# Optimization experiments

Hardware: AMD Instinct MI355X
Metric: run time of the kernel (lower is better)

Reference implementation:

```python
import jax, jax.numpy as jnp
import numpy as np

N, E, C = 50000, 10000, 500
NNZ = 400000
IN_DIM, EDGE_DIM, NODE_DIM, COMP_DIM = 128, 128, 128, 128


def _glorot(key, shape):
    fan = shape[0] + shape[1]
    return jax.random.normal(key, shape, jnp.float32) * (2.0 / fan) ** 0.5


def _seg_mean(vals, idx, num):
    # mean aggregation over segments (scatter-add + count normalize)
    s = jax.ops.segment_sum(vals, idx, num_segments=num)
    cnt = jax.ops.segment_sum(jnp.ones((idx.shape[0], 1), vals.dtype), idx, num_segments=num)
    return s / jnp.maximum(cnt, 1.0)


def _prelu(v, a):
    return jnp.where(v >= 0, v, a * v)


def _conv(x, ni, ei, ec_e, ec_c, nc_n, nc_c, n_nodes, n_edges, n_comps,
          Wne, Wen, Wec, Wnc, a):
    # node -> hyperedge message passing
    e = _seg_mean((x @ Wne)[ni], ei, n_edges)            # [E, edge_dim]
    e_act = _prelu(e, a)
    # hyperedge -> node
    n = _seg_mean((e_act @ Wen)[ei], ni, n_nodes)        # [N, node_dim]
    # edge -> component and node -> component
    c = _seg_mean((e_act @ Wec)[ec_e], ec_c, n_comps) + \
        _seg_mean((x @ Wnc)[nc_n], nc_c, n_comps)        # [C, comp_dim]
    return n, e, c


def setup_inputs() -> dict:
    key = jax.random.key(0)
    ks = jax.random.split(key, 16)
    x = jax.random.normal(ks[0], (N, IN_DIM), jnp.float32)
    hyperedge_index = jnp.stack([
        jax.random.randint(ks[1], (NNZ,), 0, N),
        jax.random.randint(ks[2], (NNZ,), 0, E),
    ])
    hyperedge_component_index = jnp.stack([
        jnp.arange(E), jax.random.randint(ks[3], (E,), 0, C)])
    node_component_index = jnp.stack([
        jnp.arange(N), jax.random.randint(ks[4], (N,), 0, C)])
    return dict(
        x=x,
        hyperedge_index=hyperedge_index,
        hyperedge_component_index=hyperedge_component_index,
        node_component_index=node_component_index,
        num_nodes=N, num_edges=E, num_components=C,
        W_ne0=_glorot(ks[5], (IN_DIM, EDGE_DIM)),
        W_en0=_glorot(ks[6], (EDGE_DIM, NODE_DIM)),
        W_ec0=_glorot(ks[7], (EDGE_DIM, COMP_DIM)),
        W_nc0=_glorot(ks[8], (IN_DIM, COMP_DIM)),
        W_ne1=_glorot(ks[9], (NODE_DIM, EDGE_DIM)),
        W_en1=_glorot(ks[10], (EDGE_DIM, NODE_DIM)),
        W_ec1=_glorot(ks[11], (EDGE_DIM, COMP_DIM)),
        W_nc1=_glorot(ks[12], (NODE_DIM, COMP_DIM)),
        prelu_a=jnp.array(0.25, jnp.float32),
    )


def reference(x, hyperedge_index, hyperedge_component_index, node_component_index,
              num_nodes, num_edges, num_components,
              W_ne0, W_en0, W_ec0, W_nc0, W_ne1, W_en1, W_ec1, W_nc1, prelu_a):
    ni, ei = hyperedge_index[0], hyperedge_index[1]
    ec_e, ec_c = hyperedge_component_index[0], hyperedge_component_index[1]
    nc_n, nc_c = node_component_index[0], node_component_index[1]
    layers = [(W_ne0, W_en0, W_ec0, W_nc0), (W_ne1, W_en1, W_ec1, W_nc1)]
    e_out = c_out = None
    for Wne, Wen, Wec, Wnc in layers:
        n_out, e_out, c_out = _conv(x, ni, ei, ec_e, ec_c, nc_n, nc_c,
                                    num_nodes, num_edges, num_components,
                                    Wne, Wen, Wec, Wnc, prelu_a)
        x = _prelu(n_out, prelu_a)  # HyperEncoder applies act between/after layers
    return (x, e_out, c_out)
```

## Files before the change

kernel.cpp:

```cpp
#include <hip/hip_runtime.h>
#include <stdint.h>

typedef unsigned int u32;
typedef _Float16 f16;
typedef f16 half8 __attribute__((ext_vector_type(8)));
typedef float f32x4 __attribute__((ext_vector_type(4)));
#define TS 4096
#define KB2 256
#define CH 2048

__device__ __forceinline__ float bflo(u32 u) { return __uint_as_float(u << 16); }
__device__ __forceinline__ float bfhi(u32 u) { return __uint_as_float(u & 0xffff0000u); }
__device__ __forceinline__ u32 f2bf(float x) {
    u32 u = __float_as_uint(x);
    return (u + 0x7fffu + ((u >> 16) & 1u)) >> 16;
}
__device__ __forceinline__ u32 pack2(float a, float b) { return f2bf(a) | (f2bf(b) << 16); }

__device__ __forceinline__ int bstart2(int b, int total) {
    return (int)(((unsigned long long)b * (u32)total + KB2 - 1) / KB2);
}

__device__ __forceinline__ int blk_exscan(int v, int& total) {
    __shared__ int ws[5];
    int t = threadIdx.x, lane = t & 63, w = t >> 6;
    int inc = v;
    for (int d = 1; d < 64; d <<= 1) { int u = __shfl_up(inc, d, 64); if (lane >= d) inc += u; }
    __syncthreads();
    if (lane == 63) ws[w] = inc;
    __syncthreads();
    if (t == 0) { int acc = 0; for (int i = 0; i < 4; ++i) { int x = ws[i]; ws[i] = acc; acc += x; } ws[4] = acc; }
    __syncthreads();
    total = ws[4];
    return ws[w] + (inc - v);
}

#define ACC8(v) do { \
    a[0] += bflo((v).x); a[1] += bfhi((v).x); a[2] += bflo((v).y); a[3] += bfhi((v).y); \
    a[4] += bflo((v).z); a[5] += bfhi((v).z); a[6] += bflo((v).w); a[7] += bfhi((v).w); } while (0)

__device__ __forceinline__ void seg_mean8(const u32* __restrict__ in,
                                          const int* __restrict__ items,
                                          const int* __restrict__ off,
                                          int nseg, int nrows, int seg, float a[8]) {
    int lane = threadIdx.x & 63;
    int rs = lane >> 4;
    int cc = lane & 15;
#pragma unroll
    for (int i = 0; i < 8; ++i) a[i] = 0.f;
    int s0 = 0, s1 = 0;
    if (seg < nseg) { s0 = off[seg]; s1 = off[seg + 1]; }
    const uint4* rows = (const uint4*)in;
    int base = s0;
    for (; base + 16 <= s1; base += 16) {
        u32 r0 = (u32)items[base + rs];
        u32 r1 = (u32)items[base + 4 + rs];
        u32 r2 = (u32)items[base + 8 + rs];
        u32 r3 = (u32)items[base + 12 + rs];
        r0 = (r0 < (u32)nrows) ? r0 : 0u;
        r1 = (r1 < (u32)nrows) ? r1 : 0u;
        r2 = (r2 < (u32)nrows) ? r2 : 0u;
        r3 = (r3 < (u32)nrows) ? r3 : 0u;
        uint4 v0 = rows[(size_t)r0 * 16 + cc];
        uint4 v1 = rows[(size_t)r1 * 16 + cc];
        uint4 v2 = rows[(size_t)r2 * 16 + cc];
        uint4 v3 = rows[(size_t)r3 * 16 + cc];
        ACC8(v0); ACC8(v1); ACC8(v2); ACC8(v3);
    }
    for (; base + 8 <= s1; base += 8) {
        u32 r0 = (u32)items[base + rs];
        u32 r1 = (u32)items[base + 4 + rs];
        r0 = (r0 < (u32)nrows) ? r0 : 0u;
        r1 = (r1 < (u32)nrows) ? r1 : 0u;
        uint4 v0 = rows[(size_t)r0 * 16 + cc];
        uint4 v1 = rows[(size_t)r1 * 16 + cc];
        ACC8(v0); ACC8(v1);
    }
    int idx = base + rs;
    if (idx < s1) {
        u32 r = (u32)items[idx]; r = (r < (u32)nrows) ? r : 0u;
        uint4 v = rows[(size_t)r * 16 + cc];
        ACC8(v);
    }
    idx += 4;
    if (idx < s1) {
        u32 r = (u32)items[idx]; r = (r < (u32)nrows) ? r : 0u;
        uint4 v = rows[(size_t)r * 16 + cc];
        ACC8(v);
    }
#pragma unroll
    for (int i = 0; i < 8; ++i) {
        a[i] += __shfl_xor(a[i], 16, 64);
        a[i] += __shfl_xor(a[i], 32, 64);
    }
    float inv = 1.f / fmaxf((float)(s1 - s0), 1.f);
#pragma unroll
    for (int i = 0; i < 8; ++i) a[i] *= inv;
}

__device__ __forceinline__ void agg4_body(const u32* __restrict__ in,
                                          const int* __restrict__ items,
                                          const int* __restrict__ off,
                                          float* __restrict__ out_f32,
                                          u32* __restrict__ out_bf,
                                          int nseg, int nrows, int do_prelu,
                                          const float* __restrict__ alpha_p, int seg) {
    if (seg >= nseg) return;
    int lane = threadIdx.x & 63;
    int rs = lane >> 4;
    int cc = lane & 15;
    float a[8];
    seg_mean8(in, items, off, nseg, nrows, seg, a);
    if (do_prelu) {
        float al = *alpha_p;
#pragma unroll
        for (int i = 0; i < 8; ++i) a[i] = (a[i] >= 0.f) ? a[i] : al * a[i];
    }
    if (rs == 0) {
        if (out_f32) {
            float* o = out_f32 + ((size_t)seg << 7) + cc * 8;
            *(float4*)o       = make_float4(a[0], a[1], a[2], a[3]);
            *(float4*)(o + 4) = make_float4(a[4], a[5], a[6], a[7]);
        }
        if (out_bf) {
            uint4 pk;
            pk.x = pack2(a[0], a[1]); pk.y = pack2(a[2], a[3]);
            pk.z = pack2(a[4], a[5]); pk.w = pack2(a[6], a[7]);
            *(uint4*)(out_bf + ((size_t)seg << 6) + cc * 4) = pk;
        }
    }
}

__global__ __launch_bounds__(256) void k_front(
        const int* __restrict__ ni, const int* __restrict__ ei,
        const int* __restrict__ nc_c, const int* __restrict__ ec_c,
        int* __restrict__ bcntE, int* __restrict__ bcntN,
        int* __restrict__ cnt_cn, int* __restrict__ cnt_ce,
        int nnz, int n, int e, int nbh,
        int* __restrict__ ticket,
        int* __restrict__ basesE, int* __restrict__ basesN,
        int* __restrict__ bcur_e, int* __restrict__ bcur_n,
        int* __restrict__ off_cn, int* __restrict__ off_ce,
        int* __restrict__ cur_cn, int* __restrict__ cur_ce, int c,
        const float* __restrict__ W0, const float* __restrict__ W1,
        const float* __restrict__ W2, const float* __restrict__ W3,
        const float* __restrict__ W4, const float* __restrict__ W5,
        f16* __restrict__ wt6) {
    int t = threadIdx.x;
    int b = blockIdx.x;
    if (b >= nbh) {
        int gid = (b - nbh) * 256 + t;
        if (gid >= 6 * 2048) return;
        int m = gid >> 11;
        int rem = gid & 2047;
        int cq = rem >> 4;
        int s = rem & 15;
        const float* W = (m == 0) ? W0 : (m == 1) ? W1 : (m == 2) ? W2 :
                         (m == 3) ? W3 : (m == 4) ? W4 : W5;
        int khi = ((s & 7) ^ (cq & 7)) | (s & 8);
        int k0 = khi << 3;
        union { f16 h[8]; uint4 v; } u;
#pragma unroll
        for (int j = 0; j < 8; ++j) u.h[j] = (f16)W[((k0 + j) << 7) + cq];
        *(uint4*)(wt6 + ((size_t)m << 14) + (cq << 7) + (s << 3)) = u.v;
        return;
    }
    __shared__ int hE[KB2], hN[KB2];
    __shared__ int lastflag;
    hE[t] = 0; hN[t] = 0;
    __syncthreads();
    int base = b * CH;
    int lim = base + CH; if (lim > nnz) lim = nnz;
    for (int i = base + t; i < lim; i += 256) {
        u32 v = (u32)ni[i], eg = (u32)ei[i];
        if (v >= (u32)n) v = 0;
        if (eg >= (u32)e) eg = 0;
        atomicAdd(&hE[(int)(((unsigned long long)eg * KB2) / (u32)e)], 1);
        atomicAdd(&hN[(int)(((unsigned long long)v  * KB2) / (u32)n)], 1);
    }
    __syncthreads();
    if (hE[t]) atomicAdd(&bcntE[t], hE[t]);
    if (hN[t]) atomicAdd(&bcntN[t], hN[t]);
    int gid = b * 256 + t, stride = nbh * 256;
    for (int j = gid; j < n + e; j += stride) {
        if (j < n) atomicAdd(&cnt_cn[nc_c[j]], 1);
        else       atomicAdd(&cnt_ce[ec_c[j - n]], 1);
    }
    __syncthreads();
    if (t == 0) {
        __threadfence();
        lastflag = (atomicAdd(ticket, 1) == nbh - 1);
    }
    __syncthreads();
    if (!lastflag) return;
    __threadfence();
    int tot;
    int v = bcntE[t];
    int ex = blk_exscan(v, tot);
    basesE[t] = ex; bcur_e[t] = ex;
    if (t == 0) basesE[KB2] = tot;
    v = bcntN[t];
    ex = blk_exscan(v, tot);
    basesN[t] = ex; bcur_n[t] = ex;
    if (t == 0) basesN[KB2] = tot;
    int i0 = 2 * t, i1 = 2 * t + 1;
    int v0 = (i0 < c) ? cnt_cn[i0] : 0;
    int v1 = (i1 < c) ? cnt_cn[i1] : 0;
    ex = blk_exscan(v0 + v1, tot);
    if (i0 < c) { off_cn[i0] = ex;      cur_cn[i0] = ex; }
    if (i1 < c) { off_cn[i1] = ex + v0; cur_cn[i1] = ex + v0; }
    if (t == 0) off_cn[c] = tot;
    v0 = (i0 < c) ? cnt_ce[i0] : 0;
    v1 = (i1 < c) ? cnt_ce[i1] : 0;
    ex = blk_exscan(v0 + v1, tot);
    if (i0 < c) { off_ce[i0] = ex;      cur_ce[i0] = ex; }
    if (i1 < c) { off_ce[i1] = ex + v0; cur_ce[i1] = ex + v0; }
    if (t == 0) off_ce[c] = tot;
}

__global__ __launch_bounds__(256) void k_part_a(
        const int* __restrict__ ni, const int* __restrict__ ei,
        int* __restrict__ bcur_e, int* __restrict__ bcur_n,
        u32* __restrict__ stg_e, u32* __restrict__ stg_n,
        const int* __restrict__ nc_n, const int* __restrict__ nc_c,
        const int* __restrict__ ec_e, const int* __restrict__ ec_c,
        int* __restrict__ cur_cn, int* __restrict__ cur_ce,
        int* __restrict__ csr_cn, int* __restrict__ csr_ce,
        const float2* __restrict__ xin, u32* __restrict__ xout, int npairs,
        int nnz, int n, int e, int nbh) {
    __shared__ u32 pk[CH];
    __shared__ unsigned short bb[CH];
    __shared__ int hist[KB2];
    __shared__ int gb[KB2];
    int t = threadIdx.x;
    int bx = blockIdx.x;
    if (bx >= 2 * nbh) {
        int j = (bx - 2 * nbh) * 256 + t;
        if (j < npairs) { float2 v = xin[j]; xout[j] = pack2(v.x, v.y); }
        return;
    }
    int side = bx >= nbh;
    int pb = side ? bx - nbh : bx;
    int base = pb * CH;
    int cnt  = nnz - base; if (cnt > CH) cnt = CH;
    for (int i = t; i < KB2; i += 256) hist[i] = 0;
    __syncthreads();
    u32 total = side ? (u32)n : (u32)e;
    for (int i = t; i < cnt; i += 256) {
        int v = ni[base + i], eg = ei[base + i];
        u32 key = side ? (u32)v : (u32)eg;
        u32 pay = side ? (u32)eg : (u32)v;
        if (key >= total) key = 0;
        u32 b = (u32)(((unsigned long long)key * KB2) / total);
        pk[i] = side ? (pay | (key << 14)) : (pay | (key << 16));
        bb[i] = (unsigned short)b;
        atomicAdd(&hist[b], 1);
    }
    __syncthreads();
    int* cursor = side ? bcur_n : bcur_e;
    u32* stg    = side ? stg_n  : stg_e;
    if (t < KB2) {
        int h = hist[t];
        gb[t] = h ? atomicAdd(&cursor[t], h) : 0;
        hist[t] = 0;
    }
    __syncthreads();
    for (int i = t; i < cnt; i += 256) {
        int b = bb[i];
        int r = atomicAdd(&hist[b], 1);
        stg[gb[b] + r] = pk[i];
    }
    int gid = pb * 256 + t;
    int stride = nbh * 256;
    if (side == 0) {
        for (int j = gid; j < e; j += stride) { int c = ec_c[j]; csr_ce[atomicAdd(&cur_ce[c], 1)] = ec_e[j]; }
    } else {
        for (int j = gid; j < n; j += stride) { int c = nc_c[j]; csr_cn[atomicAdd(&cur_cn[c], 1)] = nc_n[j]; }
    }
}

__global__ __launch_bounds__(256) void k_part_b2(
        const u32* __restrict__ stg_e, const u32* __restrict__ stg_n,
        const int* __restrict__ basesE, const int* __restrict__ basesN,
        int* __restrict__ off_e, int* __restrict__ off_n,
        int* __restrict__ csr_e, int* __restrict__ csr_n, int e, int n) {
    __shared__ int lcnt[256];
    int b = blockIdx.x, t = threadIdx.x;
    const u32* stg; const int* bases; int* off; int* csr; int total; int shift; u32 mask;
    if (b < KB2) { stg = stg_e; bases = basesE; off = off_e; csr = csr_e; total = e; shift = 16; mask = 0xFFFFu; }
    else { b -= KB2; stg = stg_n; bases = basesN; off = off_n; csr = csr_n; total = n; shift = 14; mask = 0x3FFFu; }
    int lo = bstart2(b, total), hi = bstart2(b + 1, total);
    int nid = hi - lo;
    int sbase = bases[b], send = bases[b + 1];
    lcnt[t] = 0;
    __syncthreads();
    for (int i = sbase + t; i < send; i += 256) {
        int key = (int)(stg[i] >> shift);
        atomicAdd(&lcnt[key - lo], 1);
    }
    __syncthreads();
    int cval = (t < nid) ? lcnt[t] : 0;
    int tot;
    int ex = blk_exscan(cval, tot);
    int cursor = sbase + ex;
    if (t < nid) { off[lo + t] = cursor; lcnt[t] = cursor; }
    if (t == 0 && hi == total) off[total] = send;
    __syncthreads();
    for (int i = sbase + t; i < send; i += 256) {
        u32 s = stg[i];
        int key = (int)(s >> shift);
        int pay = (int)(s & mask);
        int p = atomicAdd(&lcnt[key - lo], 1);
        csr[p] = pay;
    }
}

__global__ void k_cvt(const float2* __restrict__ in, u32* __restrict__ out, int npairs) {
    int j = blockIdx.x * blockDim.x + threadIdx.x;
    if (j < npairs) { float2 v = in[j]; out[j] = pack2(v.x, v.y); }
}

__global__ void k_hist_fb(const int* __restrict__ ni, const int* __restrict__ ei,
                          const int* __restrict__ nc_c, const int* __restrict__ ec_c,
                          int* __restrict__ deg_e, int* __restrict__ deg_n,
                          int* __restrict__ cnt_cn, int* __restrict__ cnt_ce,
                          int nnz, int n, int e) {
    int j = blockIdx.x * blockDim.x + threadIdx.x;
    if (j < nnz) {
        atomicAdd(&deg_e[ei[j]], 1);
        atomicAdd(&deg_n[ni[j]], 1);
    }
    if (j < n) atomicAdd(&cnt_cn[nc_c[j]], 1);
    if (j < e) atomicAdd(&cnt_ce[ec_c[j]], 1);
}

__device__ __forceinline__ void scan_sel(int b, int t0, int t01, int t012,
        const int* c0, int* o0, int* u0, int n0,
        const int* c1, int* o1, int* u1, int n1,
        const int* c2, int* o2, int* u2, int n2,
        const int* c3, int* o3, int* u3, int n3,
        const int*& cnt, int*& off, int*& cur, int& n, int& tile) {
    if (b < t0)        { cnt = c0; off = o0; cur = u0; n = n0; tile = b; }
    else if (b < t01)  { cnt = c1; off = o1; cur = u1; n = n1; tile = b - t0; }
    else if (b < t012) { cnt = c2; off = o2; cur = u2; n = n2; tile = b - t01; }
    else               { cnt = c3; off = o3; cur = u3; n = n3; tile = b - t012; }
}

__global__ void k_scan_p1(const int* c0, int n0, const int* c1, int n1,
                          const int* c2, int n2, const int* c3, int n3,
                          int t0, int t01, int t012, int* __restrict__ tilesum) {
    __shared__ int ws[4];
    int b = blockIdx.x;
    const int* cnt; int* off; int* cur; int n; int tile;
    scan_sel(b, t0, t01, t012, c0, nullptr, nullptr, n0, c1, nullptr, nullptr, n1,
             c2, nullptr, nullptr, n2, c3, nullptr, nullptr, n3, cnt, off, cur, n, tile);
    int base = tile * TS + threadIdx.x * 16;
    int s = 0;
#pragma unroll
    for (int i = 0; i < 16; ++i) { int idx = base + i; if (idx < n) s += cnt[idx]; }
    for (int d = 32; d; d >>= 1) s += __shfl_xor(s, d, 64);
    int lane = threadIdx.x & 63, w = threadIdx.x >> 6;
    if (lane == 0) ws[w] = s;
    __syncthreads();
    if (threadIdx.x == 0) tilesum[b] = ws[0] + ws[1] + ws[2] + ws[3];
}

__global__ void k_scan_p2(const int* __restrict__ tilesum, int* __restrict__ tilebase,
                          int t0, int t01, int t012, int t0123,
                          int* o0, int n0, int* o1, int n1, int* o2, int n2, int* o3, int n3) {
    if (threadIdx.x != 0 || blockIdx.x != 0) return;
    int carry = 0;
    for (int b = 0;    b < t0;    ++b) { tilebase[b] = carry; carry += tilesum[b]; } o0[n0] = carry;
    carry = 0;
    for (int b = t0;   b < t01;   ++b) { tilebase[b] = carry; carry += tilesum[b]; } o1[n1] = carry;
    carry = 0;
    for (int b = t01;  b < t012;  ++b) { tilebase[b] = carry; carry += tilesum[b]; } o2[n2] = carry;
    carry = 0;
    for (int b = t012; b < t0123; ++b) { tilebase[b] = carry; carry += tilesum[b]; } o3[n3] = carry;
}

__global__ void k_scan_p3(const int* c0, int* o0, int* u0, int n0,
                          const int* c1, int* o1, int* u1, int n1,
                          const int* c2, int* o2, int* u2, int n2,
                          const int* c3, int* o3, int* u3, int n3,
                          int t0, int t01, int t012, const int* __restrict__ tilebase) {
    __shared__ int wsum[4];
    int b = blockIdx.x;
    const int* cnt; int* off; int* cur; int n; int tile;
    scan_sel(b, t0, t01, t012, c0, o0, u0, n0, c1, o1, u1, n1,
             c2, o2, u2, n2, c3, o3, u3, n3, cnt, off, cur, n, tile);
    int lane = threadIdx.x & 63, w = threadIdx.x >> 6;
    int base = tile * TS + threadIdx.x * 16;
    int vals[16];
    int s = 0;
#pragma unroll
    for (int i = 0; i < 16; ++i) { int idx = base + i; int v = (idx < n) ? cnt[idx] : 0; vals[i] = v; s += v; }
    int inc = s;
    for (int d = 1; d < 64; d <<= 1) { int u = __shfl_up(inc, d, 64); if (lane >= d) inc += u; }
    if (lane == 63) wsum[w] = inc;
    __syncthreads();
    if (threadIdx.x == 0) {
        int acc = tilebase[b];
        for (int i = 0; i < 4; ++i) { int t = wsum[i]; wsum[i] = acc; acc += t; }
    }
    __syncthreads();
    int ex = wsum[w] + (inc - s);
#pragma unroll
    for (int i = 0; i < 16; ++i) {
        int idx = base + i;
        if (idx < n) { off[idx] = ex; cur[idx] = ex; }
        ex += vals[i];
    }
}

__global__ void k_scatter(const int* __restrict__ ni, const int* __restrict__ ei,
                          const int* __restrict__ nc_n, const int* __restrict__ nc_c,
                          const int* __restrict__ ec_e, const int* __restrict__ ec_c,
                          int* __restrict__ cur_e, int* __restrict__ cur_n,
                          int* __restrict__ cur_cn, int* __restrict__ cur_ce,
                          int* __restrict__ csr_e, int* __restrict__ csr_n,
                          int* __restrict__ csr_cn, int* __restrict__ csr_ce,
                          int nnz, int n, int e) {
    int j = blockIdx.x * blockDim.x + threadIdx.x;
    if (j < nnz) {
        int v = ni[j], eg = ei[j];
        csr_e[atomicAdd(&cur_e[eg], 1)] = v;
        csr_n[atomicAdd(&cur_n[v], 1)] = eg;
    }
    if (j < n) { int c = nc_c[j]; csr_cn[atomicAdd(&cur_cn[c], 1)] = nc_n[j]; }
    if (j < e) { int c = ec_c[j]; csr_ce[atomicAdd(&cur_ce[c], 1)] = ec_e[j]; }
}

__global__ __launch_bounds__(256) void k_agg4(
        const u32* __restrict__ in, const int* __restrict__ items,
        const int* __restrict__ off, float* __restrict__ out_f32,
        u32* __restrict__ out_bf,
        int nseg, int nrows, int do_prelu, const float* __restrict__ alpha_p) {
    int seg = blockIdx.x * (blockDim.x >> 6) + (threadIdx.x >> 6);
    agg4_body(in, items, off, out_f32, out_bf, nseg, nrows, do_prelu, alpha_p, seg);
}

__global__ __launch_bounds__(256) void k_agg4h(
        const u32* __restrict__ in, const int* __restrict__ items,
        const int* __restrict__ off, f16* __restrict__ outh,
        int nseg, int nrows) {
    int seg = blockIdx.x * (blockDim.x >> 6) + (threadIdx.x >> 6);
    if (seg >= nseg) return;
    float a[8];
    seg_mean8(in, items, off, nseg, nrows, seg, a);
    int lane = threadIdx.x & 63, rs = lane >> 4, cc = lane & 15;
    if (rs == 0) {
        union { f16 h[8]; uint4 v; } u;
#pragma unroll
        for (int i = 0; i < 8; ++i) u.h[i] = (f16)a[i];
        *(uint4*)(outh + ((size_t)seg << 7) + cc * 8) = u.v;
    }
}

__global__ __launch_bounds__(256) void k_agg_final(
        const u32* __restrict__ ybf, const int* __restrict__ csr_n, const int* __restrict__ off_n,
        float* __restrict__ out_x, int n, int e,
        const u32* __restrict__ eactbf, const int* __restrict__ csr_ce, const int* __restrict__ off_ce,
        float* __restrict__ ca_e,
        const u32* __restrict__ x1bf, const int* __restrict__ csr_cn, const int* __restrict__ off_cn,
        float* __restrict__ ca_n,
        int c, int nblkN, int ncb, const float* __restrict__ alpha_p) {
    int b = blockIdx.x;
    int wv = threadIdx.x >> 6;
    if (b < nblkN) {
        agg4_body(ybf, csr_n, off_n, out_x, nullptr, n, e, 1, alpha_p, b * 4 + wv);
    } else if (b < nblkN + ncb) {
        agg4_body(eactbf, csr_ce, off_ce, ca_e, nullptr, c, e, 0, nullptr, (b - nblkN) * 4 + wv);
    } else {
        agg4_body(x1bf, csr_cn, off_cn, ca_n, nullptr, c, n, 0, nullptr, (b - nblkN - ncb) * 4 + wv);
    }
}

__global__ __launch_bounds__(256) void k_mlp_mfma(
        const f16* __restrict__ Ah,
        const f16* __restrict__ W1t, const f16* __restrict__ W2t,
        float* __restrict__ out_raw, u32* __restrict__ out_actbf,
        u32* __restrict__ out_ybf, int M, const float* __restrict__ alpha_p) {
    __shared__ f16 As[32 * 128];
    __shared__ f16 Wt[128 * 128];
    int t = threadIdx.x;
    int rb = blockIdx.x * 32;
    float al = *alpha_p;
    {
        const uint4* src = (const uint4*)W1t;
        uint4* dst = (uint4*)Wt;
        for (int i = t; i < 2048; i += 256) dst[i] = src[i];
    }
    {
        const uint4* Ag = (const uint4*)Ah;
        for (int i = t; i < 512; i += 256) {
            int r = i >> 4, s = i & 15;
            int row = rb + r;
            uint4 v = make_uint4(0u, 0u, 0u, 0u);
            if (row < M) v = Ag[(size_t)row * 16 + s];
            *(uint4*)((char*)As + (r << 8) + ((s << 4) ^ ((r & 7) << 4))) = v;
        }
    }
    __syncthreads();

    int lane = t & 63, wv = t >> 6;
    int r0  = (wv >> 1) << 4;
    int ctb = (wv & 1) << 2;
    int frow = lane & 15;
    int fk = (lane >> 4) << 3;
    int rl0 = r0 + ((lane >> 4) << 2);
    int ar = r0 + frow;
    int asw = (ar & 7) << 4;

    f32x4 acc[4] = {{0.f,0.f,0.f,0.f},{0.f,0.f,0.f,0.f},{0.f,0.f,0.f,0.f},{0.f,0.f,0.f,0.f}};
#pragma unroll
    for (int ks = 0; ks < 4; ++ks) {
        int kb2 = (ks * 32 + fk) << 1;
        half8 a = *(const half8*)((const char*)As + (ar << 8) + (kb2 ^ asw));
#pragma unroll
        for (int j = 0; j < 4; ++j) {
            int c = ((ctb + j) << 4) + frow;
            half8 b = *(const half8*)((const char*)Wt + (c << 8) + (kb2 ^ ((c & 7) << 4)));
            acc[j] = __builtin_amdgcn_mfma_f32_16x16x32_f16(a, b, acc[j], 0, 0, 0);
        }
    }
    __syncthreads();
    {
        const uint4* src = (const uint4*)W2t;
        uint4* dst = (uint4*)Wt;
        for (int i = t; i < 2048; i += 256) dst[i] = src[i];
    }
#pragma unroll
    for (int j = 0; j < 4; ++j) {
        int c = ((ctb + j) << 4) + frow;
#pragma unroll
        for (int rg = 0; rg < 4; ++rg) {
            int rl = rl0 + rg;
            int row = rb + rl;
            float ev = acc[j][rg];
            if (out_raw != nullptr && row < M) out_raw[((size_t)row << 7) + c] = ev;
            float av = (ev >= 0.f) ? ev : al * ev;
            float po = __shfl_xor(av, 1, 64);
            if (out_actbf != nullptr && (frow & 1) == 0 && row < M)
                out_actbf[((size_t)row << 6) + (c >> 1)] = pack2(av, po);
            *(f16*)((char*)As + (rl << 8) + (((c << 1)) ^ ((rl & 7) << 4))) = (f16)av;
        }
    }
    __syncthreads();
    f32x4 acc2[4] = {{0.f,0.f,0.f,0.f},{0.f,0.f,0.f,0.f},{0.f,0.f,0.f,0.f},{0.f,0.f,0.f,0.f}};
#pragma unroll
    for (int ks = 0; ks < 4; ++ks) {
        int kb2 = (ks * 32 + fk) << 1;
        half8 a = *(const half8*)((const char*)As + (ar << 8) + (kb2 ^ asw));
#pragma unroll
        for (int j = 0; j < 4; ++j) {
            int c = ((ctb + j) << 4) + frow;
            half8 b = *(const half8*)((const char*)Wt + (c << 8) + (kb2 ^ ((c & 7) << 4)));
            acc2[j] = __builtin_amdgcn_mfma_f32_16x16x32_f16(a, b, acc2[j], 0, 0, 0);
        }
    }
#pragma unroll
    for (int j = 0; j < 4; ++j) {
        int c = ((ctb + j) << 4) + frow;
#pragma unroll
        for (int rg = 0; rg < 4; ++rg) {
            int rl = rl0 + rg;
            int row = rb + rl;
            float yv = acc2[j][rg];
            float po = __shfl_xor(yv, 1, 64);
            if ((frow & 1) == 0 && row < M)
                out_ybf[((size_t)row << 6) + (c >> 1)] = pack2(yv, po);
        }
    }
}

__global__ __launch_bounds__(256) void k_gemm_mfma(
        const float* __restrict__ A1, const f16* __restrict__ W1t,
        const float* __restrict__ A2, const f16* __restrict__ W2t,
        float* __restrict__ out, int M) {
    __shared__ f16 Asd[2][32 * 128];
    __shared__ f16 Wt[128 * 128];
    int t = threadIdx.x;
    int rb = blockIdx.x * 32;
    {
        const uint4* src = (const uint4*)W1t;
        uint4* dst = (uint4*)Wt;
        for (int i = t; i < 2048; i += 256) dst[i] = src[i];
    }
    for (int p = 0; p < 2; ++p) {
        const float* Ap = p ? A2 : A1;
        for (int i = t; i < 32 * 32; i += 256) {
            int r = i >> 5, dc = i & 31;
            int row = rb + r;
            float4 v = make_float4(0.f, 0.f, 0.f, 0.f);
            if (row < M) v = *(const float4*)(Ap + ((size_t)row << 7) + dc * 4);
            f16* q = (f16*)((char*)Asd[p] + (r << 8) + ((dc << 3) ^ ((r & 7) << 4)));
            q[0] = (f16)v.x; q[1] = (f16)v.y; q[2] = (f16)v.z; q[3] = (f16)v.w;
        }
    }
    __syncthreads();

    int lane = t & 63, wv = t >> 6;
    int r0  = (wv >> 1) << 4;
    int ctb = (wv & 1) << 2;
    int frow = lane & 15;
    int fk = (lane >> 4) << 3;
    int rl0 = r0 + ((lane >> 4) << 2);
    int ar = r0 + frow;
    int asw = (ar & 7) << 4;

    f32x4 acc[4] = {{0.f,0.f,0.f,0.f},{0.f,0.f,0.f,0.f},{0.f,0.f,0.f,0.f},{0.f,0.f,0.f,0.f}};
#pragma unroll
    for (int ks = 0; ks < 4; ++ks) {
        int kb2 = (ks * 32 + fk) << 1;
        half8 a = *(const half8*)((const char*)Asd[0] + (ar << 8) + (kb2 ^ asw));
#pragma unroll
        for (int j = 0; j < 4; ++j) {
            int c = ((ctb + j) << 4) + frow;
            half8 b = *(const half8*)((const char*)Wt + (c << 8) + (kb2 ^ ((c & 7) << 4)));
            acc[j] = __builtin_amdgcn_mfma_f32_16x16x32_f16(a, b, acc[j], 0, 0, 0);
        }
    }
    __syncthreads();
    {
        const uint4* src = (const uint4*)W2t;
        uint4* dst = (uint4*)Wt;
        for (int i = t; i < 2048; i += 256) dst[i] = src[i];
    }
    __syncthreads();
#pragma unroll
    for (int ks = 0; ks < 4; ++ks) {
        int kb2 = (ks * 32 + fk) << 1;
        half8 a = *(const half8*)((const char*)Asd[1] + (ar << 8) + (kb2 ^ asw));
#pragma unroll
        for (int j = 0; j < 4; ++j) {
            int c = ((ctb + j) << 4) + frow;
            half8 b = *(const half8*)((const char*)Wt + (c << 8) + (kb2 ^ ((c & 7) << 4)));
            acc[j] = __builtin_amdgcn_mfma_f32_16x16x32_f16(a, b, acc[j], 0, 0, 0);
        }
    }
#pragma unroll
    for (int j = 0; j < 4; ++j) {
        int c = ((ctb + j) << 4) + frow;
#pragma unroll
        for (int rg = 0; rg < 4; ++rg) {
            int row = rb + rl0 + rg;
            if (row < M) out[((size_t)row << 7) + c] = acc[j][rg];
        }
    }
}

extern "C" void kernel_launch(void* const* d_in, const int* in_sizes, int n_in,
                              void* d_out, int out_size, void* d_ws, size_t ws_size,
                              hipStream_t stream) {
    const int N   = in_sizes[0] / 128;
    const int NNZ = in_sizes[1] / 2;
    const int E   = in_sizes[2] / 2;
    const int C   = 500;

    const float* x0 = (const float*)d_in[0];
    const int* ni   = (const int*)d_in[1];
    const int* ei   = ni + NNZ;
    const int* ec_e = (const int*)d_in[2];
    const int* ec_c = ec_e + E;
    const int* nc_n = (const int*)d_in[3];
    const int* nc_c = nc_n + N;
    const float* Wne0 = (const float*)d_in[7];
    const float* Wen0 = (const float*)d_in[8];
    const float* Wne1 = (const float*)d_in[11];
    const float* Wen1 = (const float*)d_in[12];
    const float* Wec1 = (const float*)d_in[13];
    const float* Wnc1 = (const float*)d_in[14];
    const float* alpha = (const float*)d_in[15];

    float* out_x = (float*)d_out;
    float* out_e = out_x + (size_t)N * 128;
    float* out_c = out_e + (size_t)E * 128;

    char* w = (char*)d_ws;
    auto alloc = [&](size_t bytes) { char* p = w; w += (bytes + 255) & ~(size_t)255; return p; };
    int* zgrp   = (int*)alloc((size_t)(2 * KB2 + 2 * C + 1) * 4);
    int* bcntE  = zgrp;
    int* bcntN  = zgrp + KB2;
    int* cnt_cn = zgrp + 2 * KB2;
    int* cnt_ce = zgrp + 2 * KB2 + C;
    int* ticket = zgrp + 2 * KB2 + 2 * C;
    int* off_e  = (int*)alloc((size_t)(E + 1) * 4);
    int* off_n  = (int*)alloc((size_t)(N + 1) * 4);
    int* off_cn = (int*)alloc((size_t)(C + 1) * 4);
    int* off_ce = (int*)alloc((size_t)(C + 1) * 4);
    int* cur_cn = (int*)alloc((size_t)C * 4);
    int* cur_ce = (int*)alloc((size_t)C * 4);
    int* csr_e  = (int*)alloc((size_t)NNZ * 4);
    int* csr_n  = (int*)alloc((size_t)NNZ * 4);
    int* csr_cn = (int*)alloc((size_t)N * 4);
    int* csr_ce = (int*)alloc((size_t)E * 4);
    int* basesE = (int*)alloc((size_t)(KB2 + 1) * 4);
    int* basesN = (int*)alloc((size_t)(KB2 + 1) * 4);
    int* bcur_e = (int*)alloc(KB2 * 4);
    int* bcur_n = (int*)alloc(KB2 * 4);
    u32* stg_e  = (u32*)alloc((size_t)NNZ * 4);
    u32* stg_n  = (u32*)alloc((size_t)NNZ * 4);
    u32* xbf    = (u32*)alloc((size_t)N * 64 * 4);
    u32* x1bf   = (u32*)alloc((size_t)N * 64 * 4);
    u32* ybf    = (u32*)alloc((size_t)E * 64 * 4);
    u32* eactbf = (u32*)alloc((size_t)E * 64 * 4);
    f16* xah    = (f16*)alloc((size_t)E * 128 * 2);
    float* ca_e = (float*)alloc((size_t)C * 128 * 4);
    float* ca_n = (float*)alloc((size_t)C * 128 * 4);
    f16* wt6    = (f16*)alloc((size_t)6 * 16384 * 2);
    int* deg_e    = (int*)alloc((size_t)E * 4);
    int* deg_n    = (int*)alloc((size_t)N * 4);
    int* cur_e    = (int*)alloc((size_t)E * 4);
    int* cur_n    = (int*)alloc((size_t)N * 4);
    int* tilesum  = (int*)alloc(64 * 4);
    int* tilebase = (int*)alloc(64 * 4);

    const int th = 256;
    const int npairs = N * 64;
    const int nbh = (NNZ + CH - 1) / CH;
    const int nkc = (npairs + th - 1) / th;

    bool binned = (E <= 16384) && (N <= 65536) && (E >= KB2) && (N >= KB2) &&
                  ((N + KB2 - 1) / KB2 <= 256) && (C <= 512);
    const int nbh_eff = binned ? nbh : 0;

    hipMemsetAsync(zgrp, 0, (size_t)(2 * KB2 + 2 * C + 1) * 4, stream);
    k_front<<<nbh_eff + 48, 256, 0, stream>>>(
        ni, ei, nc_c, ec_c,
        bcntE, bcntN, cnt_cn, cnt_ce, NNZ, N, E, nbh_eff,
        ticket, basesE, basesN, bcur_e, bcur_n,
        off_cn, off_ce, cur_cn, cur_ce, C,
        Wne0, Wen0, Wne1, Wen1, Wec1, Wnc1, wt6);

    if (binned) {
        k_part_a<<<2 * nbh + nkc, 256, 0, stream>>>(
            ni, ei, bcur_e, bcur_n, stg_e, stg_n,
            nc_n, nc_c, ec_e, ec_c,
            cur_cn, cur_ce, csr_cn, csr_ce,
            (const float2*)x0, xbf, npairs, NNZ, N, E, nbh);
        k_part_b2<<<2 * KB2, 256, 0, stream>>>(stg_e, stg_n, basesE, basesN,
                                               off_e, off_n, csr_e, csr_n, E, N);
    } else {
        hipMemsetAsync(deg_e, 0, (size_t)E * 4, stream);
        hipMemsetAsync(deg_n, 0, (size_t)N * 4, stream);
        k_cvt<<<(npairs + th - 1) / th, th, 0, stream>>>((const float2*)x0, xbf, npairs);
        k_hist_fb<<<(NNZ > N + E ? NNZ : N + E) / th + 1, th, 0, stream>>>(
            ni, ei, nc_c, ec_c, deg_e, deg_n, cnt_cn, cnt_ce, NNZ, N, E);
        const int t0 = (E + TS - 1) / TS, t1 = (N + TS - 1) / TS;
        const int t2 = (C + TS - 1) / TS, t3 = (C + TS - 1) / TS;
        const int t01 = t0 + t1, t012 = t01 + t2, t0123 = t012 + t3;
        k_scan_p1<<<t0123, 256, 0, stream>>>(deg_e, E, deg_n, N, cnt_cn, C, cnt_ce, C,
                                             t0, t01, t012, tilesum);
        k_scan_p2<<<1, 64, 0, stream>>>(tilesum, tilebase, t0, t01, t012, t0123,
                                        off_e, E, off_n, N, off_cn, C, off_ce, C);
        k_scan_p3<<<t0123, 256, 0, stream>>>(deg_e, off_e, cur_e, E,
                                             deg_n, off_n, cur_n, N,
                                             cnt_cn, off_cn, cur_cn, C,
                                             cnt_ce, off_ce, cur_ce, C,
                                             t0, t01, t012, tilebase);
        k_scatter<<<(NNZ + th - 1) / th, th, 0, stream>>>(ni, ei, nc_n, nc_c, ec_e, ec_c,
                                                          cur_e, cur_n, cur_cn, cur_ce,
                                                          csr_e, csr_n, csr_cn, csr_ce, NNZ, N, E);
    }

    const int gmlp = (E + 31) / 32;
    k_agg4h<<<(E + 3) / 4, 256, 0, stream>>>(xbf, csr_e, off_e, xah, E, N);
    k_mlp_mfma<<<gmlp, 256, 0, stream>>>(xah, wt6, wt6 + 16384, nullptr, nullptr, ybf, E, alpha);
    k_agg4<<<(N + 3) / 4, 256, 0, stream>>>(ybf, csr_n, off_n, nullptr, x1bf, N, E, 1, alpha);
    k_agg4h<<<(E + 3) / 4, 256, 0, stream>>>(x1bf, csr_e, off_e, xah, E, N);
    k_mlp_mfma<<<gmlp, 256, 0, stream>>>(xah, wt6 + 2 * 16384, wt6 + 3 * 16384,
                                         out_e, eactbf, ybf, E, alpha);
    {
        const int nblkN = (N + 3) / 4;
        const int ncb   = (C + 3) / 4;
        k_agg_final<<<nblkN + 2 * ncb, 256, 0, stream>>>(
            ybf, csr_n, off_n, out_x, N, E,
            eactbf, csr_ce, off_ce, ca_e,
            x1bf,   csr_cn, off_cn, ca_n,
            C, nblkN, ncb, alpha);
    }
    k_gemm_mfma<<<(C + 31) / 32, 256, 0, stream>>>(ca_e, wt6 + 4 * 16384,
                                                   ca_n, wt6 + 5 * 16384, out_c, C);
}
```

Before: 263.2 us.

## Fuse back-half message-passing stages into one persistent cooperative kernel

Replaces the sequence of aggregation, MLP, and final GEMM launches with a single cooperative persistent kernel that loops over work items and uses grid-wide syncs between stages. It also moves the node-to-component aggregation earlier, overlapping it with the second edge aggregation, and adds nontemporal stores for the final outputs. The aim is to remove per-launch overhead and tail gaps between dependent kernels. In exchange, the grid is capped by occupancy at 4 blocks per CU, each grid.sync has a cost, and the work inside each stage loses the parallelism of a full oversubscribed launch.

```diff
diff --git a/kernel.cpp b/kernel.cpp
--- a/kernel.cpp
+++ b/kernel.cpp
@@ -1,5 +1,8 @@
 #include <hip/hip_runtime.h>
+#include <hip/hip_cooperative_groups.h>
 #include <stdint.h>
+
+namespace cg = cooperative_groups;
 
 typedef unsigned int u32;
 typedef _Float16 f16;
@@ -104,7 +107,8 @@
                                           float* __restrict__ out_f32,
                                           u32* __restrict__ out_bf,
                                           int nseg, int nrows, int do_prelu,
-                                          const float* __restrict__ alpha_p, int seg) {
+                                          const float* __restrict__ alpha_p, int seg,
+                                          int nt) {
     if (seg >= nseg) return;
     int lane = threadIdx.x & 63;
     int rs = lane >> 4;
@@ -119,8 +123,15 @@
     if (rs == 0) {
         if (out_f32) {
             float* o = out_f32 + ((size_t)seg << 7) + cc * 8;
-            *(float4*)o       = make_float4(a[0], a[1], a[2], a[3]);
-            *(float4*)(o + 4) = make_float4(a[4], a[5], a[6], a[7]);
+            f32x4 v0 = {a[0], a[1], a[2], a[3]};
+            f32x4 v1 = {a[4], a[5], a[6], a[7]};
+            if (nt) {
+                __builtin_nontemporal_store(v0, (f32x4*)o);
+                __builtin_nontemporal_store(v1, (f32x4*)(o + 4));
+            } else {
+                *(f32x4*)o = v0;
+                *(f32x4*)(o + 4) = v1;
+            }
         }
         if (out_bf) {
             uint4 pk;
@@ -129,6 +140,228 @@
             *(uint4*)(out_bf + ((size_t)seg << 6) + cc * 4) = pk;
         }
     }
+}
+
+__device__ __forceinline__ void aggh_body(const u32* __restrict__ in,
+                                          const int* __restrict__ items,
+                                          const int* __restrict__ off,
+                                          f16* __restrict__ outh,
+                                          int nseg, int nrows, int seg) {
+    if (seg >= nseg) return;
+    float a[8];
+    seg_mean8(in, items, off, nseg, nrows, seg, a);
+    int lane = threadIdx.x & 63, rs = lane >> 4, cc = lane & 15;
+    if (rs == 0) {
+        union { f16 h[8]; uint4 v; } u;
+#pragma unroll
+        for (int i = 0; i < 8; ++i) u.h[i] = (f16)a[i];
+        *(uint4*)(outh + ((size_t)seg << 7) + cc * 8) = u.v;
+    }
+}
+
+__device__ __forceinline__ void mlp_body(f16* As, f16* Wt, int rb,
+        const f16* __restrict__ Ah,
+        const f16* __restrict__ W1t, const f16* __restrict__ W2t,
+        float* __restrict__ out_raw, u32* __restrict__ out_actbf,
+        u32* __restrict__ out_ybf, int M, float al) {
+    int t = threadIdx.x;
+    __syncthreads();
+    {
+        const uint4* src = (const uint4*)W1t;
+        uint4* dst = (uint4*)Wt;
+        for (int i = t; i < 2048; i += 256) dst[i] = src[i];
+    }
+    {
+        const uint4* Ag = (const uint4*)Ah;
+        for (int i = t; i < 512; i += 256) {
+            int r = i >> 4, s = i & 15;
+            int row = rb + r;
+            uint4 v = make_uint4(0u, 0u, 0u, 0u);
+            if (row < M) v = Ag[(size_t)row * 16 + s];
+            *(uint4*)((char*)As + (r << 8) + ((s << 4) ^ ((r & 7) << 4))) = v;
+        }
+    }
+    __syncthreads();
+
+    int lane = t & 63, wv = t >> 6;
+    int r0  = (wv >> 1) << 4;
+    int ctb = (wv & 1) << 2;
+    int frow = lane & 15;
+    int fk = (lane >> 4) << 3;
+    int rl0 = r0 + ((lane >> 4) << 2);
+    int ar = r0 + frow;
+    int asw = (ar & 7) << 4;
+
+    f32x4 acc[4] = {{0.f,0.f,0.f,0.f},{0.f,0.f,0.f,0.f},{0.f,0.f,0.f,0.f},{0.f,0.f,0.f,0.f}};
+#pragma unroll
+    for (int ks = 0; ks < 4; ++ks) {
+        int kb2 = (ks * 32 + fk) << 1;
+        half8 a = *(const half8*)((const char*)As + (ar << 8) + (kb2 ^ asw));
+#pragma unroll
+        for (int j = 0; j < 4; ++j) {
+            int c = ((ctb + j) << 4) + frow;
+            half8 b = *(const half8*)((const char*)Wt + (c << 8) + (kb2 ^ ((c & 7) << 4)));
+            acc[j] = __builtin_amdgcn_mfma_f32_16x16x32_f16(a, b, acc[j], 0, 0, 0);
+        }
+    }
+    __syncthreads();
+    {
+        const uint4* src = (const uint4*)W2t;
+        uint4* dst = (uint4*)Wt;
+        for (int i = t; i < 2048; i += 256) dst[i] = src[i];
+    }
+#pragma unroll
+    for (int j = 0; j < 4; ++j) {
+        int c = ((ctb + j) << 4) + frow;
+#pragma unroll
+        for (int rg = 0; rg < 4; ++rg) {
+            int rl = rl0 + rg;
+            int row = rb + rl;
+            float ev = acc[j][rg];
+            if (out_raw != nullptr && row < M)
+                __builtin_nontemporal_store(ev, out_raw + ((size_t)row << 7) + c);
+            float av = (ev >= 0.f) ? ev : al * ev;
+            float po = __shfl_xor(av, 1, 64);
+            if (out_actbf != nullptr && (frow & 1) == 0 && row < M)
+                out_actbf[((size_t)row << 6) + (c >> 1)] = pack2(av, po);
+            *(f16*)((char*)As + (rl << 8) + (((c << 1)) ^ ((rl & 7) << 4))) = (f16)av;
+        }
+    }
+    __syncthreads();
+    f32x4 acc2[4] = {{0.f,0.f,0.f,0.f},{0.f,0.f,0.f,0.f},{0.f,0.f,0.f,0.f},{0.f,0.f,0.f,0.f}};
+#pragma unroll
+    for (int ks = 0; ks < 4; ++ks) {
+        int kb2 = (ks * 32 + fk) << 1;
+        half8 a = *(const half8*)((const char*)As + (ar << 8) + (kb2 ^ asw));
+#pragma unroll
+        for (int j = 0; j < 4; ++j) {
+            int c = ((ctb + j) << 4) + frow;
+            half8 b = *(const half8*)((const char*)Wt + (c << 8) + (kb2 ^ ((c & 7) << 4)));
+            acc2[j] = __builtin_amdgcn_mfma_f32_16x16x32_f16(a, b, acc2[j], 0, 0, 0);
+        }
+    }
+#pragma unroll
+    for (int j = 0; j < 4; ++j) {
+        int c = ((ctb + j) << 4) + frow;
+#pragma unroll
+        for (int rg = 0; rg < 4; ++rg) {
+            int rl = rl0 + rg;
+            int row = rb + rl;
+            float yv = acc2[j][rg];
+            float po = __shfl_xor(yv, 1, 64);
+            if ((frow & 1) == 0 && row < M)
+                out_ybf[((size_t)row << 6) + (c >> 1)] = pack2(yv, po);
+        }
+    }
+}
+
+__device__ __forceinline__ void gemm_body(f16* As, f16* Wt, int rb,
+        const float* __restrict__ A1, const f16* __restrict__ W1t,
+        const float* __restrict__ A2, const f16* __restrict__ W2t,
+        float* __restrict__ out, int M) {
+    int t = threadIdx.x, lane = t & 63, wv = t >> 6;
+    int r0 = (wv >> 1) << 4, ctb = (wv & 1) << 2;
+    int frow = lane & 15, fk = (lane >> 4) << 3;
+    int rl0 = r0 + ((lane >> 4) << 2);
+    int ar = r0 + frow, asw = (ar & 7) << 4;
+    f32x4 acc[4] = {{0.f,0.f,0.f,0.f},{0.f,0.f,0.f,0.f},{0.f,0.f,0.f,0.f},{0.f,0.f,0.f,0.f}};
+#pragma unroll 1
+    for (int p = 0; p < 2; ++p) {
+        const float* Ap = p ? A2 : A1;
+        const f16* Wp = p ? W2t : W1t;
+        __syncthreads();
+        {
+            const uint4* src = (const uint4*)Wp;
+            uint4* dst = (uint4*)Wt;
+            for (int i = t; i < 2048; i += 256) dst[i] = src[i];
+        }
+        for (int i = t; i < 32 * 32; i += 256) {
+            int r = i >> 5, dc = i & 31;
+            int row = rb + r;
+            float4 v = make_float4(0.f, 0.f, 0.f, 0.f);
+            if (row < M) v = *(const float4*)(Ap + ((size_t)row << 7) + dc * 4);
+            f16* q = (f16*)((char*)As + (r << 8) + ((dc << 3) ^ ((r & 7) << 4)));
+            q[0] = (f16)v.x; q[1] = (f16)v.y; q[2] = (f16)v.z; q[3] = (f16)v.w;
+        }
+        __syncthreads();
+#pragma unroll
+        for (int ks = 0; ks < 4; ++ks) {
+            int kb2 = (ks * 32 + fk) << 1;
+            half8 a = *(const half8*)((const char*)As + (ar << 8) + (kb2 ^ asw));
+#pragma unroll
+            for (int j = 0; j < 4; ++j) {
+                int c = ((ctb + j) << 4) + frow;
+                half8 b = *(const half8*)((const char*)Wt + (c << 8) + (kb2 ^ ((c & 7) << 4)));
+                acc[j] = __builtin_amdgcn_mfma_f32_16x16x32_f16(a, b, acc[j], 0, 0, 0);
+            }
+        }
+    }
+#pragma unroll
+    for (int j = 0; j < 4; ++j) {
+        int c = ((ctb + j) << 4) + frow;
+#pragma unroll
+        for (int rg = 0; rg < 4; ++rg) {
+            int row = rb + rl0 + rg;
+            if (row < M)
+                __builtin_nontemporal_store(acc[j][rg], out + ((size_t)row << 7) + c);
+        }
+    }
+}
+
+struct BackArgs {
+    const u32* xbf; u32* x1bf; u32* ybf; u32* eactbf; f16* xah;
+    const int* csr_e; const int* off_e;
+    const int* csr_n; const int* off_n;
+    const int* csr_cn; const int* off_cn;
+    const int* csr_ce; const int* off_ce;
+    const f16* wt6;
+    float* out_x; float* out_e; float* out_c;
+    float* ca_e; float* ca_n;
+    const float* alpha;
+    int N, E, C;
+};
+
+__global__ __launch_bounds__(256, 4) void k_back(BackArgs A) {
+    __shared__ f16 As[32 * 128];
+    __shared__ f16 Wt[128 * 128];
+    cg::grid_group grid = cg::this_grid();
+    int G = gridDim.x, bid = blockIdx.x;
+    int wv = threadIdx.x >> 6;
+    float al = *A.alpha;
+    const int EB = (A.E + 3) / 4, NB = (A.N + 3) / 4, CB = (A.C + 3) / 4;
+    const int GM = (A.E + 31) / 32, CG = (A.C + 31) / 32;
+
+    for (int vb = bid; vb < EB; vb += G)
+        aggh_body(A.xbf, A.csr_e, A.off_e, A.xah, A.E, A.N, vb * 4 + wv);
+    grid.sync();
+    for (int vb = bid; vb < GM; vb += G)
+        mlp_body(As, Wt, vb * 32, A.xah, A.wt6, A.wt6 + 16384,
+                 nullptr, nullptr, A.ybf, A.E, al);
+    grid.sync();
+    for (int vb = bid; vb < NB; vb += G)
+        agg4_body(A.ybf, A.csr_n, A.off_n, nullptr, A.x1bf, A.N, A.E, 1, A.alpha,
+                  vb * 4 + wv, 0);
+    grid.sync();
+    for (int vb = bid; vb < EB + CB; vb += G) {
+        if (vb < EB) aggh_body(A.x1bf, A.csr_e, A.off_e, A.xah, A.E, A.N, vb * 4 + wv);
+        else agg4_body(A.x1bf, A.csr_cn, A.off_cn, A.ca_n, nullptr, A.C, A.N, 0, A.alpha,
+                       (vb - EB) * 4 + wv, 0);
+    }
+    grid.sync();
+    for (int vb = bid; vb < GM; vb += G)
+        mlp_body(As, Wt, vb * 32, A.xah, A.wt6 + 2 * 16384, A.wt6 + 3 * 16384,
+                 A.out_e, A.eactbf, A.ybf, A.E, al);
+    grid.sync();
+    for (int vb = bid; vb < NB + CB; vb += G) {
+        if (vb < NB) agg4_body(A.ybf, A.csr_n, A.off_n, A.out_x, nullptr, A.N, A.E, 1,
+                               A.alpha, vb * 4 + wv, 1);
+        else agg4_body(A.eactbf, A.csr_ce, A.off_ce, A.ca_e, nullptr, A.C, A.E, 0,
+                       A.alpha, (vb - NB) * 4 + wv, 0);
+    }
+    grid.sync();
+    for (int vb = bid; vb < CG; vb += G)
+        gemm_body(As, Wt, vb * 32, A.ca_e, A.wt6 + 4 * 16384,
+                  A.ca_n, A.wt6 + 5 * 16384, A.out_c, A.C);
 }
 
 __global__ __launch_bounds__(256) void k_front(
@@ -437,7 +670,7 @@
         u32* __restrict__ out_bf,
         int nseg, int nrows, int do_prelu, const float* __restrict__ alpha_p) {
     int seg = blockIdx.x * (blockDim.x >> 6) + (threadIdx.x >> 6);
-    agg4_body(in, items, off, out_f32, out_bf, nseg, nrows, do_prelu, alpha_p, seg);
+    agg4_body(in, items, off, out_f32, out_bf, nseg, nrows, do_prelu, alpha_p, seg, 0);
 }
 
 __global__ __launch_bounds__(256) void k_agg4h(
@@ -445,16 +678,7 @@
         const int* __restrict__ off, f16* __restrict__ outh,
         int nseg, int nrows) {
     int seg = blockIdx.x * (blockDim.x >> 6) + (threadIdx.x >> 6);
-    if (seg >= nseg) return;
-    float a[8];
-    seg_mean8(in, items, off, nseg, nrows, seg, a);
-    int lane = threadIdx.x & 63, rs = lane >> 4, cc = lane & 15;
-    if (rs == 0) {
-        union { f16 h[8]; uint4 v; } u;
-#pragma unroll
-        for (int i = 0; i < 8; ++i) u.h[i] = (f16)a[i];
-        *(uint4*)(outh + ((size_t)seg << 7) + cc * 8) = u.v;
-    }
+    aggh_body(in, items, off, outh, nseg, nrows, seg);
 }
 
 __global__ __launch_bounds__(256) void k_agg_final(
@@ -468,11 +692,11 @@
     int b = blockIdx.x;
     int wv = threadIdx.x >> 6;
     if (b < nblkN) {
-        agg4_body(ybf, csr_n, off_n, out_x, nullptr, n, e, 1, alpha_p, b * 4 + wv);
+        agg4_body(ybf, csr_n, off_n, out_x, nullptr, n, e, 1, alpha_p, b * 4 + wv, 1);
     } else if (b < nblkN + ncb) {
-        agg4_body(eactbf, csr_ce, off_ce, ca_e, nullptr, c, e, 0, nullptr, (b - nblkN) * 4 + wv);
+        agg4_body(eactbf, csr_ce, off_ce, ca_e, nullptr, c, e, 0, nullptr, (b - nblkN) * 4 + wv, 0);
     } else {
-        agg4_body(x1bf, csr_cn, off_cn, ca_n, nullptr, c, n, 0, nullptr, (b - nblkN - ncb) * 4 + wv);
+        agg4_body(x1bf, csr_cn, off_cn, ca_n, nullptr, c, n, 0, nullptr, (b - nblkN - ncb) * 4 + wv, 0);
     }
 }
 
@@ -483,171 +707,16 @@
         u32* __restrict__ out_ybf, int M, const float* __restrict__ alpha_p) {
     __shared__ f16 As[32 * 128];
     __shared__ f16 Wt[128 * 128];
-    int t = threadIdx.x;
-    int rb = blockIdx.x * 32;
-    float al = *alpha_p;
-    {
-        const uint4* src = (const uint4*)W1t;
-        uint4* dst = (uint4*)Wt;
-        for (int i = t; i < 2048; i += 256) dst[i] = src[i];
-    }
-    {
-        const uint4* Ag = (const uint4*)Ah;
-        for (int i = t; i < 512; i += 256) {
-            int r = i >> 4, s = i & 15;
-            int row = rb + r;
-            uint4 v = make_uint4(0u, 0u, 0u, 0u);
-            if (row < M) v = Ag[(size_t)row * 16 + s];
-            *(uint4*)((char*)As + (r << 8) + ((s << 4) ^ ((r & 7) << 4))) = v;
-        }
-    }
-    __syncthreads();
-
-    int lane = t & 63, wv = t >> 6;
-    int r0  = (wv >> 1) << 4;
-    int ctb = (wv & 1) << 2;
-    int frow = lane & 15;
-    int fk = (lane >> 4) << 3;
-    int rl0 = r0 + ((lane >> 4) << 2);
-    int ar = r0 + frow;
-    int asw = (ar & 7) << 4;
-
-    f32x4 acc[4] = {{0.f,0.f,0.f,0.f},{0.f,0.f,0.f,0.f},{0.f,0.f,0.f,0.f},{0.f,0.f,0.f,0.f}};
-#pragma unroll
-    for (int ks = 0; ks < 4; ++ks) {
-        int kb2 = (ks * 32 + fk) << 1;
-        half8 a = *(const half8*)((const char*)As + (ar << 8) + (kb2 ^ asw));
-#pragma unroll
-        for (int j = 0; j < 4; ++j) {
-            int c = ((ctb + j) << 4) + frow;
-            half8 b = *(const half8*)((const char*)Wt + (c << 8) + (kb2 ^ ((c & 7) << 4)));
-            acc[j] = __builtin_amdgcn_mfma_f32_16x16x32_f16(a, b, acc[j], 0, 0, 0);
-        }
-    }
-    __syncthreads();
-    {
-        const uint4* src = (const uint4*)W2t;
-        uint4* dst = (uint4*)Wt;
-        for (int i = t; i < 2048; i += 256) dst[i] = src[i];
-    }
-#pragma unroll
-    for (int j = 0; j < 4; ++j) {
-        int c = ((ctb + j) << 4) + frow;
-#pragma unroll
-        for (int rg = 0; rg < 4; ++rg) {
-            int rl = rl0 + rg;
-            int row = rb + rl;
-            float ev = acc[j][rg];
-            if (out_raw != nullptr && row < M) out_raw[((size_t)row << 7) + c] = ev;
-            float av = (ev >= 0.f) ? ev : al * ev;
-            float po = __shfl_xor(av, 1, 64);
-            if (out_actbf != nullptr && (frow & 1) == 0 && row < M)
-                out_actbf[((size_t)row << 6) + (c >> 1)] = pack2(av, po);
-            *(f16*)((char*)As + (rl << 8) + (((c << 1)) ^ ((rl & 7) << 4))) = (f16)av;
-        }
-    }
-    __syncthreads();
-    f32x4 acc2[4] = {{0.f,0.f,0.f,0.f},{0.f,0.f,0.f,0.f},{0.f,0.f,0.f,0.f},{0.f,0.f,0.f,0.f}};
-#pragma unroll
-    for (int ks = 0; ks < 4; ++ks) {
-        int kb2 = (ks * 32 + fk) << 1;
-        half8 a = *(const half8*)((const char*)As + (ar << 8) + (kb2 ^ asw));
-#pragma unroll
-        for (int j = 0; j < 4; ++j) {
-            int c = ((ctb + j) << 4) + frow;
-            half8 b = *(const half8*)((const char*)Wt + (c << 8) + (kb2 ^ ((c & 7) << 4)));
-            acc2[j] = __builtin_amdgcn_mfma_f32_16x16x32_f16(a, b, acc2[j], 0, 0, 0);
-        }
-    }
-#pragma unroll
-    for (int j = 0; j < 4; ++j) {
-        int c = ((ctb + j) << 4) + frow;
-#pragma unroll
-        for (int rg = 0; rg < 4; ++rg) {
-            int rl = rl0 + rg;
-            int row = rb + rl;
-            float yv = acc2[j][rg];
-            float po = __shfl_xor(yv, 1, 64);
-            if ((frow & 1) == 0 && row < M)
-                out_ybf[((size_t)row << 6) + (c >> 1)] = pack2(yv, po);
-        }
-    }
+    mlp_body(As, Wt, blockIdx.x * 32, Ah, W1t, W2t, out_raw, out_actbf, out_ybf, M, *alpha_p);
 }
 
 __global__ __launch_bounds__(256) void k_gemm_mfma(
         const float* __restrict__ A1, const f16* __restrict__ W1t,
         const float* __restrict__ A2, const f16* __restrict__ W2t,
         float* __restrict__ out, int M) {
-    __shared__ f16 Asd[2][32 * 128];
+    __shared__ f16 As[32 * 128];
     __shared__ f16 Wt[128 * 128];
-    int t = threadIdx.x;
-    int rb = blockIdx.x * 32;
-    {
-        const uint4* src = (const uint4*)W1t;
-        uint4* dst = (uint4*)Wt;
-        for (int i = t; i < 2048; i += 256) dst[i] = src[i];
-    }
-    for (int p = 0; p < 2; ++p) {
-        const float* Ap = p ? A2 : A1;
-        for (int i = t; i < 32 * 32; i += 256) {
-            int r = i >> 5, dc = i & 31;
-            int row = rb + r;
-            float4 v = make_float4(0.f, 0.f, 0.f, 0.f);
-            if (row < M) v = *(const float4*)(Ap + ((size_t)row << 7) + dc * 4);
-            f16* q = (f16*)((char*)Asd[p] + (r << 8) + ((dc << 3) ^ ((r & 7) << 4)));
-            q[0] = (f16)v.x; q[1] = (f16)v.y; q[2] = (f16)v.z; q[3] = (f16)v.w;
-        }
-    }
-    __syncthreads();
-
-    int lane = t & 63, wv = t >> 6;
-    int r0  = (wv >> 1) << 4;
-    int ctb = (wv & 1) << 2;
-    int frow = lane & 15;
-    int fk = (lane >> 4) << 3;
-    int rl0 = r0 + ((lane >> 4) << 2);
-    int ar = r0 + frow;
-    int asw = (ar & 7) << 4;
-
-    f32x4 acc[4] = {{0.f,0.f,0.f,0.f},{0.f,0.f,0.f,0.f},{0.f,0.f,0.f,0.f},{0.f,0.f,0.f,0.f}};
-#pragma unroll
-    for (int ks = 0; ks < 4; ++ks) {
-        int kb2 = (ks * 32 + fk) << 1;
-        half8 a = *(const half8*)((const char*)Asd[0] + (ar << 8) + (kb2 ^ asw));
-#pragma unroll
-        for (int j = 0; j < 4; ++j) {
-            int c = ((ctb + j) << 4) + frow;
-            half8 b = *(const half8*)((const char*)Wt + (c << 8) + (kb2 ^ ((c & 7) << 4)));
-            acc[j] = __builtin_amdgcn_mfma_f32_16x16x32_f16(a, b, acc[j], 0, 0, 0);
-        }
-    }
-    __syncthreads();
-    {
-        const uint4* src = (const uint4*)W2t;
-        uint4* dst = (uint4*)Wt;
-        for (int i = t; i < 2048; i += 256) dst[i] = src[i];
-    }
-    __syncthreads();
-#pragma unroll
-    for (int ks = 0; ks < 4; ++ks) {
-        int kb2 = (ks * 32 + fk) << 1;
-        half8 a = *(const half8*)((const char*)Asd[1] + (ar << 8) + (kb2 ^ asw));
-#pragma unroll
-        for (int j = 0; j < 4; ++j) {
-            int c = ((ctb + j) << 4) + frow;
-            half8 b = *(const half8*)((const char*)Wt + (c << 8) + (kb2 ^ ((c & 7) << 4)));
-            acc[j] = __builtin_amdgcn_mfma_f32_16x16x32_f16(a, b, acc[j], 0, 0, 0);
-        }
-    }
-#pragma unroll
-    for (int j = 0; j < 4; ++j) {
-        int c = ((ctb + j) << 4) + frow;
-#pragma unroll
-        for (int rg = 0; rg < 4; ++rg) {
-            int row = rb + rl0 + rg;
-            if (row < M) out[((size_t)row << 7) + c] = acc[j][rg];
-        }
-    }
+    gemm_body(As, Wt, blockIdx.x * 32, A1, W1t, A2, W2t, out, M);
 }
 
 extern "C" void kernel_launch(void* const* d_in, const int* in_sizes, int n_in,
@@ -764,22 +833,55 @@
                                                           csr_e, csr_n, csr_cn, csr_ce, NNZ, N, E);
     }
 
-    const int gmlp = (E + 31) / 32;
-    k_agg4h<<<(E + 3) / 4, 256, 0, stream>>>(xbf, csr_e, off_e, xah, E, N);
-    k_mlp_mfma<<<gmlp, 256, 0, stream>>>(xah, wt6, wt6 + 16384, nullptr, nullptr, ybf, E, alpha);
-    k_agg4<<<(N + 3) / 4, 256, 0, stream>>>(ybf, csr_n, off_n, nullptr, x1bf, N, E, 1, alpha);
-    k_agg4h<<<(E + 3) / 4, 256, 0, stream>>>(x1bf, csr_e, off_e, xah, E, N);
-    k_mlp_mfma<<<gmlp, 256, 0, stream>>>(xah, wt6 + 2 * 16384, wt6 + 3 * 16384,
-                                         out_e, eactbf, ybf, E, alpha);
-    {
-        const int nblkN = (N + 3) / 4;
-        const int ncb   = (C + 3) / 4;
-        k_agg_final<<<nblkN + 2 * ncb, 256, 0, stream>>>(
-            ybf, csr_n, off_n, out_x, N, E,
-            eactbf, csr_ce, off_ce, ca_e,
-            x1bf,   csr_cn, off_cn, ca_n,
-            C, nblkN, ncb, alpha);
-    }
-    k_gemm_mfma<<<(C + 31) / 32, 256, 0, stream>>>(ca_e, wt6 + 4 * 16384,
-                                                   ca_n, wt6 + 5 * 16384, out_c, C);
-}
+    static int coopG = -1;
+    if (coopG < 0) {
+        int dev = 0, sup = 0, ncu = 0, nb = 0;
+        hipGetDevice(&dev);
+        hipDeviceGetAttribute(&sup, hipDeviceAttributeCooperativeLaunch, dev);
+        hipDeviceGetAttribute(&ncu, hipDeviceAttributeMultiprocessorCount, dev);
+        hipError_t oe = hipOccupancyMaxActiveBlocksPerMultiprocessor(
+            &nb, (const void*)k_back, 256, 0);
+        coopG = (sup && oe == hipSuccess && nb > 0 && ncu > 0) ? nb * ncu : 0;
+    }
+
+    bool ran_coop = false;
+    if (coopG > 0) {
+        BackArgs ba;
+        ba.xbf = xbf; ba.x1bf = x1bf; ba.ybf = ybf; ba.eactbf = eactbf; ba.xah = xah;
+        ba.csr_e = csr_e; ba.off_e = off_e;
+        ba.csr_n = csr_n; ba.off_n = off_n;
+        ba.csr_cn = csr_cn; ba.off_cn = off_cn;
+        ba.csr_ce = csr_ce; ba.off_ce = off_ce;
+        ba.wt6 = wt6;
+        ba.out_x = out_x; ba.out_e = out_e; ba.out_c = out_c;
+        ba.ca_e = ca_e; ba.ca_n = ca_n;
+        ba.alpha = alpha;
+        ba.N = N; ba.E = E; ba.C = C;
+        void* kp[] = { (void*)&ba };
+        hipError_t le = hipLaunchCooperativeKernel((const void*)k_back,
+                                                   dim3(coopG), dim3(256), kp, 0, stream);
+        if (le == hipSuccess) ran_coop = true;
+        else coopG = 0;
+    }
+
+    if (!ran_coop) {
+        const int gmlp = (E + 31) / 32;
+        k_agg4h<<<(E + 3) / 4, 256, 0, stream>>>(xbf, csr_e, off_e, xah, E, N);
+        k_mlp_mfma<<<gmlp, 256, 0, stream>>>(xah, wt6, wt6 + 16384, nullptr, nullptr, ybf, E, alpha);
+        k_agg4<<<(N + 3) / 4, 256, 0, stream>>>(ybf, csr_n, off_n, nullptr, x1bf, N, E, 1, alpha);
+        k_agg4h<<<(E + 3) / 4, 256, 0, stream>>>(x1bf, csr_e, off_e, xah, E, N);
+        k_mlp_mfma<<<gmlp, 256, 0, stream>>>(xah, wt6 + 2 * 16384, wt6 + 3 * 16384,
+                                             out_e, eactbf, ybf, E, alpha);
+        {
+            const int nblkN = (N + 3) / 4;
+            const int ncb   = (C + 3) / 4;
+            k_agg_final<<<nblkN + 2 * ncb, 256, 0, stream>>>(
+                ybf, csr_n, off_n, out_x, N, E,
+                eactbf, csr_ce, off_ce, ca_e,
+                x1bf,   csr_cn, off_cn, ca_n,
+                C, nblkN, ncb, alpha);
+        }
+        k_gemm_mfma<<<(C + 31) / 32, 256, 0, stream>>>(ca_e, wt6 + 4 * 16384,
+                                                       ca_n, wt6 + 5 * 16384, out_c, C);
+    }
+}
```

After: 722.2 us. 174% more time.
